# Kernel optimization log

Hardware: AMD Instinct MI355X
Metric: run time of the kernel (lower is better)

The kernel has to match this reference:

```python
import jax, jax.numpy as jnp
import numpy as np

N = 8192
IN_F = 128
OUT_F = 64
NEG_SLOPE = 0.2


def setup_inputs() -> dict:
    key = jax.random.key(0)
    k1, k2, k3, k4 = jax.random.split(key, 4)
    x = jax.random.normal(k1, (N, IN_F), dtype=jnp.float32)
    adj = jax.random.randint(k2, (N, N), 0, 2, dtype=jnp.int32)
    W = jax.random.normal(k3, (IN_F, OUT_F), dtype=jnp.float32) * (1.414 / np.sqrt(IN_F))
    a = jax.random.normal(k4, (2 * OUT_F, 1), dtype=jnp.float32) * 0.5
    return {"x": x, "adj": adj, "W": W, "a": a}


def reference(x, adj, W, a):
    # Wh: [N, F]
    Wh = x @ W
    # Decomposed pairwise score: e_ij = leaky_relu(Wh_i . a1 + Wh_j . a2)
    # identical math to the original [N*N, 2F] concat @ a construction.
    a1 = a[:OUT_F, 0]   # [F]
    a2 = a[OUT_F:, 0]   # [F]
    s1 = Wh @ a1        # [N]
    s2 = Wh @ a2        # [N]
    e = jax.nn.leaky_relu(s1[:, None] + s2[None, :], negative_slope=NEG_SLOPE)  # [N, N]
    # NOTE: the original zeros out non-edges (NOT -inf) before softmax.
    att = jnp.where(adj > 0, e, jnp.zeros_like(e))
    att = jax.nn.softmax(att, axis=1)
    return att @ Wh  # [N, F]
```

## Files before the change

### kernel.cpp

```cpp
#include <hip/hip_runtime.h>
#include <hip/hip_bf16.h>

#define N_NODES 8192
#define IN_FEAT 128
#define OUT_FEAT 64
#define NEG_SLOPE 0.2f
#define TILES (N_NODES / 16)
#define CCH 2
#define COLS (N_NODES / CCH)
#define SUBC 512
#define NSUB (COLS / SUBC)
#define KPW 4
#define ROWPAD 520
#define BUFSZ (16 * ROWPAD)
#define LOG2E 1.44269504088896340736f

using f32x4  = __attribute__((ext_vector_type(4))) float;
using i32x4  = __attribute__((ext_vector_type(4))) int;
using bf16x8 = __attribute__((ext_vector_type(8))) short;

static __device__ __forceinline__ short f2bf(float f) {
    unsigned int u = __float_as_uint(f);
    unsigned int r = (u + 0x7FFFu + ((u >> 16) & 1u)) >> 16;
    return (short)r;
}

static __device__ __forceinline__ short f2bf_fast(float f) {
    __hip_bfloat16 h = __float2bfloat16(f);
    return __builtin_bit_cast(short, h);
}

static __device__ __forceinline__ float exp2_fast(float x) {
    return __builtin_amdgcn_exp2f(x);
}

__global__ __launch_bounds__(256) void k_wh(
    const float* __restrict__ x, const float* __restrict__ W,
    const float* __restrict__ a,
    float* __restrict__ s1, float* __restrict__ s2,
    unsigned short* __restrict__ whb)
{
    __shared__ float xs[4][IN_FEAT];
    const int wv   = threadIdx.x >> 6;
    const int lane = threadIdx.x & 63;
    const int row  = blockIdx.x * 4 + wv;

    const float2 xv = *(const float2*)(x + (size_t)row * IN_FEAT + lane * 2);
    xs[wv][lane * 2]     = xv.x;
    xs[wv][lane * 2 + 1] = xv.y;
    __syncthreads();

    float acc = 0.f;
    #pragma unroll
    for (int k = 0; k < IN_FEAT; ++k)
        acc = fmaf(xs[wv][k], W[k * OUT_FEAT + lane], acc);

    float p1 = acc * a[lane];
    float p2 = acc * a[OUT_FEAT + lane];
    #pragma unroll
    for (int off = 32; off; off >>= 1) {
        p1 += __shfl_xor(p1, off);
        p2 += __shfl_xor(p2, off);
    }
    if (lane == 0) {
        s1[row] = p1 * LOG2E;
        s2[row] = p2 * LOG2E;
    }

    const int jb = row >> 5;
    const int ri = row & 31;
    const int gl = ri >> 3;
    const int e  = ri & 7;
    const int fg = lane >> 4;
    const int cl = lane & 15;
    whb[(((size_t)(jb * 4 + fg) * 64) + (gl * 16 + cl)) * 8 + e] = (unsigned short)f2bf(acc);
}

__global__ __launch_bounds__(256, 4) void k_fused(
    const int* __restrict__ adj, const float* __restrict__ s1v,
    const float* __restrict__ s2v, const unsigned short* __restrict__ whb,
    float* __restrict__ pnum, float* __restrict__ pz)
{
    __shared__ __align__(16) char lds[2 * BUFSZ + 256];
    char*  bufs = lds;
    float* zl   = (float*)(lds + 2 * BUFSZ);
    float* red  = (float*)lds;

    const int lane = threadIdx.x & 63;
    const int w    = threadIdx.x >> 6;
    const int tile = blockIdx.x;
    const int cidx = blockIdx.y;
    const int c0   = cidx * COLS;
    const int cl = lane & 15, g = lane >> 4;
    const int row = tile * 16 + cl;
    const float s1r = s1v[row];

    const int* stg = adj + ((size_t)(tile * 16 + w * 4)) * N_NODES + c0 + lane * 4;

    f32x4 acc0 = {0.f, 0.f, 0.f, 0.f};
    f32x4 acc1 = acc0, acc2 = acc0, acc3 = acc0;
    float zacc = 0.f;

    {
        i32x4 ld[8];
        #pragma unroll
        for (int rr = 0; rr < 4; ++rr)
            #pragma unroll
            for (int q = 0; q < 2; ++q)
                ld[rr * 2 + q] = __builtin_nontemporal_load(
                    (const i32x4*)(stg + (size_t)rr * N_NODES + q * 256));
        #pragma unroll
        for (int rr = 0; rr < 4; ++rr)
            #pragma unroll
            for (int q = 0; q < 2; ++q) {
                i32x4 v = ld[rr * 2 + q];
                unsigned int d = (v[0] > 0 ? 1u : 0u) | (v[1] > 0 ? 0x100u : 0u)
                               | (v[2] > 0 ? 0x10000u : 0u) | (v[3] > 0 ? 0x1000000u : 0u);
                *(unsigned int*)(bufs + (w * 4 + rr) * ROWPAD + q * 256 + lane * 4) = d;
            }
        __syncthreads();
    }

    for (int c = 0; c < NSUB; ++c) {
        const char* rbuf = bufs + (c & 1) * BUFSZ;
        const bool more = (c + 1 < NSUB);

        i32x4 ld[8];
        if (more) {
            #pragma unroll
            for (int rr = 0; rr < 4; ++rr)
                #pragma unroll
                for (int q = 0; q < 2; ++q)
                    ld[rr * 2 + q] = __builtin_nontemporal_load(
                        (const i32x4*)(stg + (size_t)rr * N_NODES + (c + 1) * SUBC + q * 256));
        }
        __builtin_amdgcn_sched_barrier(0);

        #pragma unroll
        for (int kk = 0; kk < KPW; ++kk) {
            const int ks = w * KPW + kk;
            const uint2 ab = *(const uint2*)(rbuf + cl * ROWPAD + ks * 32 + 8 * g);
            const float* sp = s2v + c0 + c * SUBC + ks * 32 + 8 * g;
            const f32x4 s0  = *(const f32x4*)(sp);
            const f32x4 s1x = *(const f32x4*)(sp + 4);
            const unsigned short* wq =
                whb + ((size_t)(c0 / 32 + c * 16 + ks)) * 2048 + lane * 8;
            bf16x8 B0 = *(const bf16x8*)(wq);
            bf16x8 B1 = *(const bf16x8*)(wq + 512);
            bf16x8 B2 = *(const bf16x8*)(wq + 1024);
            bf16x8 B3 = *(const bf16x8*)(wq + 1536);

            bf16x8 af;
            #pragma unroll
            for (int e = 0; e < 4; ++e) {
                float tv = s1r + s0[e];
                float el = fmaxf(tv, NEG_SLOPE * tv);
                float wv = ((ab.x >> (8 * e)) & 1u) ? exp2_fast(el) : 1.0f;
                zacc += wv;
                af[e] = f2bf_fast(wv);
            }
            #pragma unroll
            for (int e = 0; e < 4; ++e) {
                float tv = s1r + s1x[e];
                float el = fmaxf(tv, NEG_SLOPE * tv);
                float wv = ((ab.y >> (8 * e)) & 1u) ? exp2_fast(el) : 1.0f;
                zacc += wv;
                af[4 + e] = f2bf_fast(wv);
            }

            acc0 = __builtin_amdgcn_mfma_f32_16x16x32_bf16(af, B0, acc0, 0, 0, 0);
            acc1 = __builtin_amdgcn_mfma_f32_16x16x32_bf16(af, B1, acc1, 0, 0, 0);
            acc2 = __builtin_amdgcn_mfma_f32_16x16x32_bf16(af, B2, acc2, 0, 0, 0);
            acc3 = __builtin_amdgcn_mfma_f32_16x16x32_bf16(af, B3, acc3, 0, 0, 0);
        }

        if (more) {
            char* wbuf = bufs + ((c + 1) & 1) * BUFSZ;
            #pragma unroll
            for (int rr = 0; rr < 4; ++rr)
                #pragma unroll
                for (int q = 0; q < 2; ++q) {
                    i32x4 v = ld[rr * 2 + q];
                    unsigned int d = (v[0] > 0 ? 1u : 0u) | (v[1] > 0 ? 0x100u : 0u)
                                   | (v[2] > 0 ? 0x10000u : 0u) | (v[3] > 0 ? 0x1000000u : 0u);
                    *(unsigned int*)(wbuf + (w * 4 + rr) * ROWPAD + q * 256 + lane * 4) = d;
                }
        }
        __syncthreads();
    }

    *(f32x4*)(red + ((size_t)(w * 64 + lane)) * 16 + 0)  = acc0;
    *(f32x4*)(red + ((size_t)(w * 64 + lane)) * 16 + 4)  = acc1;
    *(f32x4*)(red + ((size_t)(w * 64 + lane)) * 16 + 8)  = acc2;
    *(f32x4*)(red + ((size_t)(w * 64 + lane)) * 16 + 12) = acc3;
    float zz = zacc + __shfl_xor(zacc, 16);
    zz += __shfl_xor(zz, 32);
    if (lane < 16) zl[w * 16 + lane] = zz;
    __syncthreads();

    f32x4 rs = {0.f, 0.f, 0.f, 0.f};
    #pragma unroll
    for (int w2 = 0; w2 < 4; ++w2)
        rs += *(const f32x4*)(red + ((size_t)(w2 * 64 + lane)) * 16 + 4 * w);

    float* pb = pnum + ((size_t)cidx * TILES + tile) * 16 * 64 + lane;
    #pragma unroll
    for (int q = 0; q < 4; ++q) pb[(w * 4 + q) * 64] = rs[q];

    if (w == 0 && lane < 16) {
        float z = zl[lane] + zl[16 + lane] + zl[32 + lane] + zl[48 + lane];
        pz[(size_t)cidx * N_NODES + tile * 16 + lane] = z;
    }
}

__global__ __launch_bounds__(64) void k_out(
    const float* __restrict__ pnum, const float* __restrict__ pz,
    float* __restrict__ out)
{
    const int lane = threadIdx.x;
    const int tile = blockIdx.x;
    const int nt   = blockIdx.y;
    const int g = lane >> 4, cli = lane & 15;

    float acc[4] = {0.f, 0.f, 0.f, 0.f};
    float zz[4]  = {0.f, 0.f, 0.f, 0.f};
    #pragma unroll
    for (int c = 0; c < CCH; ++c) {
        const float* pb = pnum + (((size_t)c * TILES + tile) * 16 + nt * 4) * 64 + lane;
        #pragma unroll
        for (int q = 0; q < 4; ++q) acc[q] += pb[q * 64];
        const float* zb = pz + (size_t)c * N_NODES + tile * 16 + g * 4;
        #pragma unroll
        for (int q = 0; q < 4; ++q) zz[q] += zb[q];
    }
    #pragma unroll
    for (int q = 0; q < 4; ++q) {
        const int node = tile * 16 + g * 4 + q;
        out[(size_t)node * OUT_FEAT + nt * 16 + cli] = acc[q] / zz[q];
    }
}

extern "C" void kernel_launch(void* const* d_in, const int* in_sizes, int n_in,
                              void* d_out, int out_size, void* d_ws, size_t ws_size,
                              hipStream_t stream) {
    const float* x   = (const float*)d_in[0];
    const int*   adj = (const int*)d_in[1];
    const float* W   = (const float*)d_in[2];
    const float* a   = (const float*)d_in[3];
    float* out = (float*)d_out;

    char* ws = (char*)d_ws;
    float* s1 = (float*)(ws);
    float* s2 = (float*)(ws + 32 * 1024);
    unsigned short* whb = (unsigned short*)(ws + 64 * 1024);
    float* pnum = (float*)(ws + 2u * 1024 * 1024);
    float* pz   = (float*)(ws + 8u * 1024 * 1024);

    k_wh   <<<dim3(N_NODES / 4), dim3(256), 0, stream>>>(x, W, a, s1, s2, whb);
    k_fused<<<dim3(TILES, CCH), dim3(256), 0, stream>>>(adj, s1, s2, whb, pnum, pz);
    k_out  <<<dim3(TILES, 4), dim3(64), 0, stream>>>(pnum, pz, out);
}
```

Baseline: 90.45 us.

## Deepen adj prefetch pipeline, stage s2 in LDS, and widen row padding

Restructures the main loop into issue/pack/compute stages. The global load of adjacency chunk c+2 is in flight while chunk c+1 is packed and chunk c is computed, so the adj stream runs two steps ahead instead of one. The s2 slice for this column chunk is copied into LDS once up front, replacing repeated global reads. The LDS row pad changes from 520 to 528 bytes, and __syncthreads is replaced by an explicit lgkmcnt wait plus s_barrier. The cost is about twice the LDS per block, which may limit occupancy, and more live registers from the deeper prefetch.

```diff
diff --git a/kernel.cpp b/kernel.cpp
--- a/kernel.cpp
+++ b/kernel.cpp
@@ -11,7 +11,7 @@
 #define SUBC 512
 #define NSUB (COLS / SUBC)
 #define KPW 4
-#define ROWPAD 520
+#define ROWPAD 528
 #define BUFSZ (16 * ROWPAD)
 #define LOG2E 1.44269504088896340736f
 
@@ -81,9 +81,10 @@
     const float* __restrict__ s2v, const unsigned short* __restrict__ whb,
     float* __restrict__ pnum, float* __restrict__ pz)
 {
-    __shared__ __align__(16) char lds[2 * BUFSZ + 256];
+    __shared__ __align__(16) char lds[2 * BUFSZ + COLS * 4 + 256];
     char*  bufs = lds;
-    float* zl   = (float*)(lds + 2 * BUFSZ);
+    float* s2l  = (float*)(lds + 2 * BUFSZ);
+    float* zl   = (float*)(lds + 2 * BUFSZ + COLS * 4);
     float* red  = (float*)lds;
 
     const int lane = threadIdx.x & 63;
@@ -97,18 +98,18 @@
 
     const int* stg = adj + ((size_t)(tile * 16 + w * 4)) * N_NODES + c0 + lane * 4;
 
-    f32x4 acc0 = {0.f, 0.f, 0.f, 0.f};
-    f32x4 acc1 = acc0, acc2 = acc0, acc3 = acc0;
-    float zacc = 0.f;
-
-    {
-        i32x4 ld[8];
+    i32x4 ld[8];
+
+    auto issue = [&](int c) {
         #pragma unroll
         for (int rr = 0; rr < 4; ++rr)
             #pragma unroll
             for (int q = 0; q < 2; ++q)
                 ld[rr * 2 + q] = __builtin_nontemporal_load(
-                    (const i32x4*)(stg + (size_t)rr * N_NODES + q * 256));
+                    (const i32x4*)(stg + (size_t)rr * N_NODES + c * SUBC + q * 256));
+    };
+    auto pack = [&](int c) {
+        char* wbuf = bufs + (c & 1) * BUFSZ;
         #pragma unroll
         for (int rr = 0; rr < 4; ++rr)
             #pragma unroll
@@ -116,31 +117,21 @@
                 i32x4 v = ld[rr * 2 + q];
                 unsigned int d = (v[0] > 0 ? 1u : 0u) | (v[1] > 0 ? 0x100u : 0u)
                                | (v[2] > 0 ? 0x10000u : 0u) | (v[3] > 0 ? 0x1000000u : 0u);
-                *(unsigned int*)(bufs + (w * 4 + rr) * ROWPAD + q * 256 + lane * 4) = d;
+                *(unsigned int*)(wbuf + (w * 4 + rr) * ROWPAD + q * 256 + lane * 4) = d;
             }
-        __syncthreads();
-    }
-
-    for (int c = 0; c < NSUB; ++c) {
+    };
+
+    f32x4 acc0 = {0.f, 0.f, 0.f, 0.f};
+    f32x4 acc1 = acc0, acc2 = acc0, acc3 = acc0;
+    float zacc = 0.f;
+
+    auto compute = [&](int c) {
         const char* rbuf = bufs + (c & 1) * BUFSZ;
-        const bool more = (c + 1 < NSUB);
-
-        i32x4 ld[8];
-        if (more) {
-            #pragma unroll
-            for (int rr = 0; rr < 4; ++rr)
-                #pragma unroll
-                for (int q = 0; q < 2; ++q)
-                    ld[rr * 2 + q] = __builtin_nontemporal_load(
-                        (const i32x4*)(stg + (size_t)rr * N_NODES + (c + 1) * SUBC + q * 256));
-        }
-        __builtin_amdgcn_sched_barrier(0);
-
         #pragma unroll
         for (int kk = 0; kk < KPW; ++kk) {
             const int ks = w * KPW + kk;
             const uint2 ab = *(const uint2*)(rbuf + cl * ROWPAD + ks * 32 + 8 * g);
-            const float* sp = s2v + c0 + c * SUBC + ks * 32 + 8 * g;
+            const float* sp = s2l + c * SUBC + ks * 32 + 8 * g;
             const f32x4 s0  = *(const f32x4*)(sp);
             const f32x4 s1x = *(const f32x4*)(sp + 4);
             const unsigned short* wq =
@@ -173,20 +164,33 @@
             acc2 = __builtin_amdgcn_mfma_f32_16x16x32_bf16(af, B2, acc2, 0, 0, 0);
             acc3 = __builtin_amdgcn_mfma_f32_16x16x32_bf16(af, B3, acc3, 0, 0, 0);
         }
-
-        if (more) {
-            char* wbuf = bufs + ((c + 1) & 1) * BUFSZ;
-            #pragma unroll
-            for (int rr = 0; rr < 4; ++rr)
-                #pragma unroll
-                for (int q = 0; q < 2; ++q) {
-                    i32x4 v = ld[rr * 2 + q];
-                    unsigned int d = (v[0] > 0 ? 1u : 0u) | (v[1] > 0 ? 0x100u : 0u)
-                                   | (v[2] > 0 ? 0x10000u : 0u) | (v[3] > 0 ? 0x1000000u : 0u);
-                    *(unsigned int*)(wbuf + (w * 4 + rr) * ROWPAD + q * 256 + lane * 4) = d;
-                }
-        }
-        __syncthreads();
+    };
+
+    {
+        const float* src = s2v + c0 + threadIdx.x * 4;
+        float* dst = s2l + threadIdx.x * 4;
+        #pragma unroll
+        for (int i = 0; i < 4; ++i)
+            *(f32x4*)(dst + i * 1024) = *(const f32x4*)(src + i * 1024);
+    }
+    issue(0);
+    pack(0);
+    issue(1);
+    __builtin_amdgcn_sched_barrier(0);
+    asm volatile("s_waitcnt lgkmcnt(0)" ::: "memory");
+    __builtin_amdgcn_s_barrier();
+    __builtin_amdgcn_sched_barrier(0);
+
+    for (int c = 0; c < NSUB; ++c) {
+        if (c + 1 < NSUB) pack(c + 1);
+        __builtin_amdgcn_sched_barrier(0);
+        if (c + 2 < NSUB) issue(c + 2);
+        __builtin_amdgcn_sched_barrier(0);
+        compute(c);
+        __builtin_amdgcn_sched_barrier(0);
+        asm volatile("s_waitcnt lgkmcnt(0)" ::: "memory");
+        __builtin_amdgcn_s_barrier();
+        __builtin_amdgcn_sched_barrier(0);
     }
 
     *(f32x4*)(red + ((size_t)(w * 64 + lane)) * 16 + 0)  = acc0;
```

Result: faster. 87.51 us (-3.3%).
